# Performance work log

Measured on AMD Instinct MI355X. Metric: run time of the kernel, lower is better.

Reference implementation:

```python
import jax, jax.numpy as jnp
import numpy as np

# Dimensions
B, S, F, PATCH, D, H, NL, DFF, HOR = 512, 336, 12, 6, 512, 8, 6, 2048, 24
NP = S // PATCH        # 56 temporal patches
DH = D // H            # head dim = 64
EPS = 1e-5


def layer_norm(x, g, b):
    m = jnp.mean(x, axis=-1, keepdims=True)
    v = jnp.mean(jnp.square(x - m), axis=-1, keepdims=True)
    return (x - m) * jax.lax.rsqrt(v + EPS) * g + b


def alibi_bias(n_heads, n):
    # slopes = 2^(-8h/H), h = 1..H (standard ALiBi, H power of 2)
    slopes = 2.0 ** (-8.0 * jnp.arange(1, n_heads + 1, dtype=jnp.float32) / n_heads)
    pos = jnp.arange(n, dtype=jnp.float32)
    dist = jnp.abs(pos[:, None] - pos[None, :])         # [n, n]
    return -slopes[:, None, None] * dist                # [H, n, n]


def setup_inputs() -> dict:
    key = jax.random.key(0)
    ks = jax.random.split(key, 16)
    g = lambda k, shape: jax.random.normal(k, shape, dtype=jnp.float32) * 0.02
    return {
        "x": jax.random.normal(ks[0], (B, S, F), dtype=jnp.float32),
        "patch_W": g(ks[1], (PATCH * F, D)),
        "patch_b": jnp.zeros((D,), jnp.float32),
        "pos": g(ks[2], (NP, D)),
        "ln1_g": jnp.ones((NL, D), jnp.float32),
        "ln1_b": jnp.zeros((NL, D), jnp.float32),
        "Wq": g(ks[3], (NL, D, D)), "bq": jnp.zeros((NL, D), jnp.float32),
        "Wk": g(ks[4], (NL, D, D)), "bk": jnp.zeros((NL, D), jnp.float32),
        "Wv": g(ks[5], (NL, D, D)), "bv": jnp.zeros((NL, D), jnp.float32),
        "Wo": g(ks[6], (NL, D, D)), "bo": jnp.zeros((NL, D), jnp.float32),
        "ln2_g": jnp.ones((NL, D), jnp.float32),
        "ln2_b": jnp.zeros((NL, D), jnp.float32),
        "W1": g(ks[7], (NL, D, DFF)), "b1": jnp.zeros((NL, DFF), jnp.float32),
        "W2": g(ks[8], (NL, DFF, D)), "b2": jnp.zeros((NL, D), jnp.float32),
        "fn_g": jnp.ones((D,), jnp.float32),
        "fn_b": jnp.zeros((D,), jnp.float32),
        "head_W": g(ks[9], (D, HOR)),
        "head_b": jnp.zeros((HOR,), jnp.float32),
    }


def reference(x, patch_W, patch_b, pos, ln1_g, ln1_b, Wq, bq, Wk, bk, Wv, bv,
              Wo, bo, ln2_g, ln2_b, W1, b1, W2, b2, fn_g, fn_b, head_W, head_b):
    # Temporal patch embedding: (B,S,F) -> (B,NP,PATCH*F) -> Linear -> +pos
    h = x.reshape(B, NP, PATCH * F) @ patch_W + patch_b + pos  # [B, NP, D]
    bias = alibi_bias(H, NP)                                   # [H, NP, NP]
    scale = 1.0 / np.sqrt(DH).astype(np.float32)
    for l in range(NL):
        # Pre-LN multi-head attention with ALiBi temporal decay bias
        hn = layer_norm(h, ln1_g[l], ln1_b[l])
        q = (hn @ Wq[l] + bq[l]).reshape(B, NP, H, DH)
        k = (hn @ Wk[l] + bk[l]).reshape(B, NP, H, DH)
        v = (hn @ Wv[l] + bv[l]).reshape(B, NP, H, DH)
        sc = jnp.einsum('bqhd,bkhd->bhqk', q, k) * scale + bias[None]
        a = jax.nn.softmax(sc, axis=-1)
        o = jnp.einsum('bhqk,bkhd->bqhd', a, v).reshape(B, NP, D)
        h = h + (o @ Wo[l] + bo[l])
        # Pre-LN feedforward
        hn2 = layer_norm(h, ln2_g[l], ln2_b[l])
        h = h + (jax.nn.gelu(hn2 @ W1[l] + b1[l]) @ W2[l] + b2[l])
    pooled = jnp.mean(h, axis=1)                               # [B, D]
    out = layer_norm(pooled, fn_g, fn_b) @ head_W + head_b     # [B, HOR]
    return out
```

## Files before the change

### kernel.cpp

```cpp
#include <hip/hip_runtime.h>
#include <hip/hip_bf16.h>
#include <math.h>

#define D_      512
#define NPATCH  56
#define DFF_    2048
#define NLAYER  6
#define HEADS   8
#define DH_     64
#define HOR_    24
#define BATCH_  512
#define NTOK_   (BATCH_ * NPATCH)
#define KPAD    96

typedef __hip_bfloat16 bf16;
typedef __bf16 bf16x8 __attribute__((ext_vector_type(8)));
typedef float  f32x4  __attribute__((ext_vector_type(4)));

__device__ __forceinline__ void gload_lds16(const void* g, void* lds) {
    __builtin_amdgcn_global_load_lds(
        (const __attribute__((address_space(1))) unsigned int*)g,
        (__attribute__((address_space(3))) unsigned int*)lds, 16, 0, 0);
}

__device__ __forceinline__ float block_sum256(float v) {
    __shared__ float sm[4];
    const int lane = threadIdx.x & 63;
    const int w    = threadIdx.x >> 6;
    #pragma unroll
    for (int o = 32; o > 0; o >>= 1) v += __shfl_down(v, o);
    __syncthreads();
    if (lane == 0) sm[w] = v;
    __syncthreads();
    return sm[0] + sm[1] + sm[2] + sm[3];
}

__device__ __forceinline__ float gelu_fast(float xg) {
    const float e = __expf(1.5957691216057308f * (xg + 0.044715f * xg * xg * xg));
    return xg - xg * __builtin_amdgcn_rcpf(1.f + e);
}

__global__ __launch_bounds__(256) void transpose_bf16_k(
    const float* __restrict__ in, bf16* __restrict__ out, int R, int C,
    size_t in_ls, size_t out_ls)
{
    __shared__ float t[32][33];
    in  += (size_t)blockIdx.z * in_ls;
    out += (size_t)blockIdx.z * out_ls;
    const int c0 = blockIdx.x * 32, r0 = blockIdx.y * 32;
    const int x = threadIdx.x & 31, y = threadIdx.x >> 5;
    #pragma unroll
    for (int i = 0; i < 4; i++)
        t[y + i * 8][x] = in[(size_t)(r0 + y + i * 8) * C + c0 + x];
    __syncthreads();
    #pragma unroll
    for (int i = 0; i < 4; i++)
        out[(size_t)(c0 + y + i * 8) * R + r0 + x] = __float2bfloat16(t[x][y + i * 8]);
}

__global__ __launch_bounds__(256) void pwt_k(
    const float* __restrict__ W, bf16* __restrict__ out)
{
    const int idx = blockIdx.x * 256 + threadIdx.x;
    if (idx >= D_ * KPAD) return;
    const int n = idx / KPAD, kk = idx % KPAD;
    out[idx] = (kk < 72) ? __float2bfloat16(W[kk * D_ + n]) : __float2bfloat16(0.f);
}

__global__ __launch_bounds__(256) void xpad_k(
    const float* __restrict__ x, bf16* __restrict__ out)
{
    const size_t idx = (size_t)blockIdx.x * 256 + threadIdx.x;
    if (idx >= (size_t)NTOK_ * KPAD) return;
    const size_t row = idx / KPAD;
    const int kk = (int)(idx - row * KPAD);
    out[idx] = (kk < 72) ? __float2bfloat16(x[row * 72 + kk]) : __float2bfloat16(0.f);
}

__global__ __launch_bounds__(256) void bqkv_k(
    const float* __restrict__ bq, const float* __restrict__ bk,
    const float* __restrict__ bv, float* __restrict__ o)
{
    const int idx = blockIdx.x * 256 + threadIdx.x;
    if (idx >= NLAYER * 3 * D_) return;
    const int l = idx / (3 * D_), n = idx % (3 * D_);
    float v;
    if      (n < D_)     v = bq[l * D_ + n];
    else if (n < 2 * D_) v = bk[l * D_ + n - D_];
    else                 v = bv[l * D_ + n - 2 * D_];
    o[idx] = v;
}

__global__ __launch_bounds__(256) void layernorm_bf16_k(
    const bf16* __restrict__ x, const float* __restrict__ g,
    const float* __restrict__ b, bf16* __restrict__ y)
{
    const int w = threadIdx.x >> 6, lane = threadIdx.x & 63;
    const size_t row = (size_t)blockIdx.x * 4 + w;
    const bf16x8 a8 = *(const bf16x8*)((const __bf16*)x + row * D_ + lane * 8);
    float a[8];
    #pragma unroll
    for (int i = 0; i < 8; i++) a[i] = (float)a8[i];
    float s = 0.f;
    #pragma unroll
    for (int i = 0; i < 8; i++) s += a[i];
    #pragma unroll
    for (int o = 32; o > 0; o >>= 1) s += __shfl_xor(s, o);
    const float mean = s * (1.f / 512.f);
    float d[8];
    #pragma unroll
    for (int i = 0; i < 8; i++) d[i] = a[i] - mean;
    float v = 0.f;
    #pragma unroll
    for (int i = 0; i < 8; i++) v += d[i] * d[i];
    #pragma unroll
    for (int o = 32; o > 0; o >>= 1) v += __shfl_xor(v, o);
    const float rstd = rsqrtf(v * (1.f / 512.f) + 1e-5f);
    const float4 g0 = *(const float4*)(g + lane * 8);
    const float4 g1 = *(const float4*)(g + lane * 8 + 4);
    const float4 b0 = *(const float4*)(b + lane * 8);
    const float4 b1 = *(const float4*)(b + lane * 8 + 4);
    const float gg[8] = {g0.x, g0.y, g0.z, g0.w, g1.x, g1.y, g1.z, g1.w};
    const float bb[8] = {b0.x, b0.y, b0.z, b0.w, b1.x, b1.y, b1.z, b1.w};
    bf16x8 o8;
    #pragma unroll
    for (int i = 0; i < 8; i++) o8[i] = (__bf16)(d[i] * rstd * gg[i] + bb[i]);
    *(bf16x8*)((__bf16*)y + row * D_ + lane * 8) = o8;
}

template<bool GELU, bool RESID, bool POS, bool QKVSPLIT>
__global__ __launch_bounds__(256, 2) void gemm_bf16_k(
    const bf16* __restrict__ A, const bf16* __restrict__ Bt,
    const float* __restrict__ bias, const bf16* __restrict__ resid,
    const float* __restrict__ pos, bf16* __restrict__ Cp,
    bf16* __restrict__ vt, int M, int N, int K, int nx)
{
    __shared__ __align__(16) bf16 As[3][128 * 32];
    __shared__ __align__(16) bf16 Bs[3][256 * 32];
    const int tid  = threadIdx.x;
    const int wid  = tid >> 6;
    const int lane = tid & 63;

    const int nwg = gridDim.x;
    const int q8 = nwg >> 3, r8 = nwg & 7;
    const int xcd = blockIdx.x & 7, idx8 = blockIdx.x >> 3;
    const int swz = (xcd < r8 ? xcd * (q8 + 1) : r8 * (q8 + 1) + (xcd - r8) * q8) + idx8;
    const int n0 = (swz % nx) * 256;
    const int m0 = (swz / nx) * 128;
    const int wr = wid >> 1, wc = wid & 1;

    f32x4 acc[4][8];
    #pragma unroll
    for (int m = 0; m < 4; m++)
        #pragma unroll
        for (int n = 0; n < 8; n++) acc[m][n] = f32x4{0.f, 0.f, 0.f, 0.f};

    const int srow = lane >> 2;
    const int schunk = ((lane & 3) ^ ((lane >> 3) & 3)) * 8;
    const bf16* gA = A  + (size_t)(m0 + wid * 32 + srow) * K + schunk;
    const bf16* gB = Bt + (size_t)(n0 + wid * 64 + srow) * K + schunk;
    const size_t k16 = (size_t)16 * K;
    const int sa0 = (wid * 2) * 512;
    const int sb0 = (wid * 4) * 512;

    const int fr = lane & 15;
    const int qg = lane >> 4;
    const int roff = fr * 32 + ((qg ^ ((fr >> 1) & 3)) * 8);

    const int nt = K >> 5;
    #define STAGE(buf, kt)  do { const bf16* _a = gA + ((kt) << 5);              \
        const bf16* _b = gB + ((kt) << 5);                                       \
        gload_lds16(_a,            &As[buf][sa0]);                               \
        gload_lds16(_a + k16,      &As[buf][sa0 + 512]);                         \
        gload_lds16(_b,            &Bs[buf][sb0]);                               \
        gload_lds16(_b + k16,      &Bs[buf][sb0 + 512]);                         \
        gload_lds16(_b + 2 * k16,  &Bs[buf][sb0 + 1024]);                        \
        gload_lds16(_b + 3 * k16,  &Bs[buf][sb0 + 1536]); } while (0)

    STAGE(0, 0);
    STAGE(1, 1);

    int cur = 0, nxt = 2;
    for (int t = 0; t < nt; t++) {
        if (t < nt - 1) asm volatile("s_waitcnt vmcnt(6)" ::: "memory");
        else            asm volatile("s_waitcnt vmcnt(0)" ::: "memory");
        __builtin_amdgcn_s_barrier();
        __builtin_amdgcn_sched_barrier(0);
        bf16x8 af[4], bg[8];
        #pragma unroll
        for (int m = 0; m < 4; m++) af[m] = *(const bf16x8*)&As[cur][(wr * 4 + m) * 512 + roff];
        #pragma unroll
        for (int n = 0; n < 8; n++) bg[n] = *(const bf16x8*)&Bs[cur][(wc * 8 + n) * 512 + roff];
        if (t + 2 < nt) STAGE(nxt, t + 2);
        #pragma unroll
        for (int m = 0; m < 4; m++)
            #pragma unroll
            for (int n = 0; n < 8; n++)
                acc[m][n] = __builtin_amdgcn_mfma_f32_16x16x32_bf16(af[m], bg[n], acc[m][n], 0, 0, 0);
        cur = (cur == 2) ? 0 : cur + 1;
        nxt = (nxt == 2) ? 0 : nxt + 1;
    }
    #undef STAGE

    const int rq = qg * 4;
    #pragma unroll
    for (int m = 0; m < 4; m++) {
        #pragma unroll
        for (int n = 0; n < 8; n++) {
            const int col = n0 + wc * 128 + n * 16 + fr;
            const float bcol = bias[col];
            #pragma unroll
            for (int j = 0; j < 4; j++) {
                const int row = m0 + wr * 64 + m * 16 + rq + j;
                float c = acc[m][n][j] + bcol;
                if (GELU)  c = gelu_fast(c);
                if (RESID) c += __bfloat162float(resid[(size_t)row * N + col]);
                if (POS)   c += pos[(size_t)(row % NPATCH) * D_ + col];
                if (QKVSPLIT) {
                    if (col < 1024) {
                        Cp[(size_t)row * 1024 + col] = __float2bfloat16(c);
                    } else {
                        const int c2 = col - 1024, hh = c2 >> 6, dd = c2 & 63;
                        const int bb = row / NPATCH, pp = row - bb * NPATCH;
                        vt[(((size_t)bb * 8 + hh) * 64 + dd) * 64 + pp] = __float2bfloat16(c);
                    }
                } else {
                    Cp[(size_t)row * N + col] = __float2bfloat16(c);
                }
            }
        }
    }
}

__global__ __launch_bounds__(256) void attn_mfma_k(
    const bf16* __restrict__ qk, const bf16* __restrict__ vt,
    bf16* __restrict__ ao)
{
    __shared__ __align__(16) bf16 St[4][64 * 72];
    const int tid  = threadIdx.x;
    const int w    = tid >> 6, lane = tid & 63;
    const int bh   = blockIdx.x * 4 + w;
    const int b    = bh >> 3, hh = bh & 7;
    const int fr   = lane & 15;
    const int qg   = lane >> 4;
    const int kc   = qg * 8;

    const bf16* Qb = qk + (size_t)b * NPATCH * 1024 + hh * 64;
    const bf16* Kb = Qb + 512;
    const bf16* Vb = vt + (size_t)bh * 4096;

    bf16x8 qf[4][2], kf[4][2];
    #pragma unroll
    for (int m = 0; m < 4; m++)
        #pragma unroll
        for (int ks = 0; ks < 2; ks++) {
            qf[m][ks] = *(const bf16x8*)&Qb[(size_t)(m * 16 + fr) * 1024 + ks * 32 + kc];
            kf[m][ks] = *(const bf16x8*)&Kb[(size_t)(m * 16 + fr) * 1024 + ks * 32 + kc];
        }

    f32x4 acc[4][4];
    #pragma unroll
    for (int m = 0; m < 4; m++)
        #pragma unroll
        for (int n = 0; n < 4; n++) acc[m][n] = f32x4{0.f, 0.f, 0.f, 0.f};
    #pragma unroll
    for (int ks = 0; ks < 2; ks++)
        #pragma unroll
        for (int m = 0; m < 4; m++)
            #pragma unroll
            for (int n = 0; n < 4; n++)
                acc[m][n] = __builtin_amdgcn_mfma_f32_16x16x32_bf16(qf[m][ks], kf[n][ks], acc[m][n], 0, 0, 0);

    bf16x8 vf[4][2];
    #pragma unroll
    for (int n = 0; n < 4; n++)
        #pragma unroll
        for (int ks = 0; ks < 2; ks++)
            vf[n][ks] = *(const bf16x8*)&Vb[(size_t)(n * 16 + fr) * 64 + ks * 32 + kc];

    const float slope = exp2f(-(float)(hh + 1));
    bf16* Sw = St[w];
    #pragma unroll
    for (int m = 0; m < 4; m++) {
        #pragma unroll
        for (int j = 0; j < 4; j++) {
            const int r = m * 16 + qg * 4 + j;
            float s[4];
            #pragma unroll
            for (int n = 0; n < 4; n++) {
                const int col = n * 16 + fr;
                float sv = acc[m][n][j] * 0.125f - slope * fabsf((float)(r - col));
                s[n] = (col >= NPATCH) ? -1e30f : sv;
            }
            float mx = fmaxf(fmaxf(s[0], s[1]), fmaxf(s[2], s[3]));
            mx = fmaxf(mx, __shfl_xor(mx, 1));
            mx = fmaxf(mx, __shfl_xor(mx, 2));
            mx = fmaxf(mx, __shfl_xor(mx, 4));
            mx = fmaxf(mx, __shfl_xor(mx, 8));
            float p[4], sum = 0.f;
            #pragma unroll
            for (int n = 0; n < 4; n++) { p[n] = __expf(s[n] - mx); sum += p[n]; }
            sum += __shfl_xor(sum, 1);
            sum += __shfl_xor(sum, 2);
            sum += __shfl_xor(sum, 4);
            sum += __shfl_xor(sum, 8);
            const float inv = 1.f / sum;
            #pragma unroll
            for (int n = 0; n < 4; n++)
                Sw[r * 72 + n * 16 + fr] = __float2bfloat16(p[n] * inv);
        }
    }

    #pragma unroll
    for (int m = 0; m < 4; m++)
        #pragma unroll
        for (int n = 0; n < 4; n++) acc[m][n] = f32x4{0.f, 0.f, 0.f, 0.f};
    #pragma unroll
    for (int m = 0; m < 4; m++)
        #pragma unroll
        for (int ks = 0; ks < 2; ks++) {
            const bf16x8 pf = *(const bf16x8*)&Sw[(m * 16 + fr) * 72 + ks * 32 + kc];
            #pragma unroll
            for (int n = 0; n < 4; n++)
                acc[m][n] = __builtin_amdgcn_mfma_f32_16x16x32_bf16(pf, vf[n][ks], acc[m][n], 0, 0, 0);
        }

    bf16* Ob = ao + (size_t)b * NPATCH * 512 + hh * 64;
    #pragma unroll
    for (int m = 0; m < 4; m++)
        #pragma unroll
        for (int j = 0; j < 4; j++) {
            const int r = m * 16 + qg * 4 + j;
            if (r < NPATCH)
                #pragma unroll
                for (int n = 0; n < 4; n++)
                    Ob[(size_t)r * 512 + n * 16 + fr] = __float2bfloat16(acc[m][n][j]);
        }
}

__global__ __launch_bounds__(256) void head_k(
    const bf16* __restrict__ h, const float* __restrict__ g,
    const float* __restrict__ bb, const float* __restrict__ hW,
    const float* __restrict__ hb, float* __restrict__ out)
{
    const int b = blockIdx.x;
    __shared__ float row[D_];
    const int tid = threadIdx.x;
    float v0 = 0.f, v1 = 0.f;
    #pragma unroll
    for (int p = 0; p < NPATCH; p++) {
        const bf16* hr = h + (size_t)b * NPATCH * D_ + (size_t)p * D_;
        v0 += __bfloat162float(hr[tid]);
        v1 += __bfloat162float(hr[tid + 256]);
    }
    v0 *= (1.f / (float)NPATCH);
    v1 *= (1.f / (float)NPATCH);
    const float mean = block_sum256(v0 + v1) * (1.f / 512.f);
    const float d0 = v0 - mean, d1 = v1 - mean;
    const float var = block_sum256(d0 * d0 + d1 * d1) * (1.f / 512.f);
    const float rstd = rsqrtf(var + 1e-5f);
    row[tid]       = d0 * rstd * g[tid]       + bb[tid];
    row[tid + 256] = d1 * rstd * g[tid + 256] + bb[tid + 256];
    __syncthreads();
    if (tid < HOR_) {
        float acc = hb[tid];
        for (int kk = 0; kk < D_; kk++) acc = fmaf(row[kk], hW[kk * HOR_ + tid], acc);
        out[(size_t)b * HOR_ + tid] = acc;
    }
}

extern "C" void kernel_launch(void* const* d_in, const int* in_sizes, int n_in,
                              void* d_out, int out_size, void* d_ws, size_t ws_size,
                              hipStream_t stream)
{
    const float* x       = (const float*)d_in[0];
    const float* patch_W = (const float*)d_in[1];
    const float* patch_b = (const float*)d_in[2];
    const float* pos     = (const float*)d_in[3];
    const float* ln1_g   = (const float*)d_in[4];
    const float* ln1_b   = (const float*)d_in[5];
    const float* Wq      = (const float*)d_in[6];
    const float* bq      = (const float*)d_in[7];
    const float* Wk      = (const float*)d_in[8];
    const float* bk      = (const float*)d_in[9];
    const float* Wv      = (const float*)d_in[10];
    const float* bv      = (const float*)d_in[11];
    const float* Wo      = (const float*)d_in[12];
    const float* bo      = (const float*)d_in[13];
    const float* ln2_g   = (const float*)d_in[14];
    const float* ln2_b   = (const float*)d_in[15];
    const float* W1      = (const float*)d_in[16];
    const float* b1      = (const float*)d_in[17];
    const float* W2      = (const float*)d_in[18];
    const float* b2      = (const float*)d_in[19];
    const float* fn_g    = (const float*)d_in[20];
    const float* fn_b    = (const float*)d_in[21];
    const float* head_W  = (const float*)d_in[22];
    const float* head_b  = (const float*)d_in[23];
    float* out = (float*)d_out;

    const size_t WELEM  = (size_t)D_ * D_;
    const size_t WFELEM = (size_t)D_ * DFF_;
    bf16* wqkvt = (bf16*)d_ws;
    bf16* wot   = wqkvt + (size_t)NLAYER * 3 * WELEM;
    bf16* w1t   = wot   + (size_t)NLAYER * WELEM;
    bf16* w2t   = w1t   + (size_t)NLAYER * WFELEM;
    bf16* pwt   = w2t   + (size_t)NLAYER * WFELEM;
    float* bqkv = (float*)(pwt + (size_t)D_ * KPAD);
    bf16* xpad  = (bf16*)(bqkv + NLAYER * 3 * D_);
    char* wend  = (char*)(xpad + (size_t)NTOK_ * KPAD);
    const size_t FIXED = (size_t)(wend - (char*)d_ws);

    int BC = 16;
    for (int cand = BATCH_; cand >= 16; cand >>= 1) {
        const size_t need = FIXED + (size_t)cand * (56 * 5120 + 65536);
        if (need <= ws_size) { BC = cand; break; }
    }
    const int nChunks = BATCH_ / BC;
    const int CT = BC * NPATCH;
    const size_t TD = (size_t)CT * D_;

    bf16* h    = (bf16*)wend;
    bf16* hn   = h + TD;
    bf16* qk   = hn + TD;
    bf16* ao   = qk + (size_t)CT * 1024;
    bf16* vt   = ao + TD;
    bf16* mid  = qk;

    transpose_bf16_k<<<dim3(16, 16, NLAYER), 256, 0, stream>>>(
        Wq, wqkvt,                 D_, D_, WELEM, 3 * WELEM);
    transpose_bf16_k<<<dim3(16, 16, NLAYER), 256, 0, stream>>>(
        Wk, wqkvt + WELEM,         D_, D_, WELEM, 3 * WELEM);
    transpose_bf16_k<<<dim3(16, 16, NLAYER), 256, 0, stream>>>(
        Wv, wqkvt + 2 * WELEM,     D_, D_, WELEM, 3 * WELEM);
    transpose_bf16_k<<<dim3(16, 16, NLAYER), 256, 0, stream>>>(
        Wo, wot,                   D_, D_, WELEM, WELEM);
    transpose_bf16_k<<<dim3(64, 16, NLAYER), 256, 0, stream>>>(
        W1, w1t,                   D_, DFF_, WFELEM, WFELEM);
    transpose_bf16_k<<<dim3(16, 64, NLAYER), 256, 0, stream>>>(
        W2, w2t,                   DFF_, D_, WFELEM, WFELEM);
    pwt_k<<<(D_ * KPAD + 255) / 256, 256, 0, stream>>>(patch_W, pwt);
    bqkv_k<<<(NLAYER * 3 * D_ + 255) / 256, 256, 0, stream>>>(bq, bk, bv, bqkv);
    xpad_k<<<((size_t)NTOK_ * KPAD + 255) / 256, 256, 0, stream>>>(x, xpad);

    const int mt  = CT / 128;
    const int g1n = (D_ / 256) * mt;
    const int gqn = (3 * D_ / 256) * mt;
    const int g2n = (DFF_ / 256) * mt;

    for (int c = 0; c < nChunks; c++) {
        const size_t tok0 = (size_t)c * CT;

        gemm_bf16_k<false, false, true, false><<<g1n, 256, 0, stream>>>(
            xpad + tok0 * KPAD, pwt, patch_b, nullptr, pos, h, nullptr,
            CT, D_, KPAD, D_ / 256);

        for (int l = 0; l < NLAYER; l++) {
            layernorm_bf16_k<<<CT / 4, 256, 0, stream>>>(h, ln1_g + l * D_, ln1_b + l * D_, hn);
            gemm_bf16_k<false, false, false, true><<<gqn, 256, 0, stream>>>(
                hn, wqkvt + (size_t)l * 3 * WELEM, bqkv + l * 3 * D_, nullptr, nullptr,
                qk, vt, CT, 3 * D_, D_, 3 * D_ / 256);
            attn_mfma_k<<<BC * 2, 256, 0, stream>>>(qk, vt, ao);
            gemm_bf16_k<false, true, false, false><<<g1n, 256, 0, stream>>>(
                ao, wot + (size_t)l * WELEM, bo + l * D_, h, nullptr, h, nullptr,
                CT, D_, D_, D_ / 256);
            layernorm_bf16_k<<<CT / 4, 256, 0, stream>>>(h, ln2_g + l * D_, ln2_b + l * D_, hn);
            gemm_bf16_k<true, false, false, false><<<g2n, 256, 0, stream>>>(
                hn, w1t + (size_t)l * WFELEM, b1 + l * DFF_, nullptr, nullptr,
                mid, nullptr, CT, DFF_, D_, DFF_ / 256);
            gemm_bf16_k<false, true, false, false><<<g1n, 256, 0, stream>>>(
                mid, w2t + (size_t)l * WFELEM, b2 + l * D_, h, nullptr, h, nullptr,
                CT, D_, DFF_, D_ / 256);
        }

        head_k<<<BC, 256, 0, stream>>>(h, fn_g, fn_b, head_W, head_b,
                                       out + (size_t)c * BC * HOR_);
    }
}
```

Measured before the change: 2.004 ms.

## Use 8-wave GEMM workgroups with 64x64 warp tiles and unified LDS staging

The GEMM goes from 4 waves to 8 waves per 128x256 block. Each wave now computes a 64x64 sub-tile instead of 64x128, which halves the accumulator registers per wave. The A and B tiles are merged into one LDS buffer, and each wave issues 3 async global-to-LDS loads per stage instead of 6. The goal is more resident waves for latency hiding; the cost is lower per-wave operand reuse from LDS and more LDS read traffic relative to MFMA work.

```diff
diff --git a/kernel.cpp b/kernel.cpp
--- a/kernel.cpp
+++ b/kernel.cpp
@@ -129,14 +129,13 @@
 }
 
 template<bool GELU, bool RESID, bool POS, bool QKVSPLIT>
-__global__ __launch_bounds__(256, 2) void gemm_bf16_k(
+__global__ __launch_bounds__(512, 4) void gemm_bf16_k(
     const bf16* __restrict__ A, const bf16* __restrict__ Bt,
     const float* __restrict__ bias, const bf16* __restrict__ resid,
     const float* __restrict__ pos, bf16* __restrict__ Cp,
     bf16* __restrict__ vt, int M, int N, int K, int nx)
 {
-    __shared__ __align__(16) bf16 As[3][128 * 32];
-    __shared__ __align__(16) bf16 Bs[3][256 * 32];
+    __shared__ __align__(16) bf16 ABs[3][384 * 32];
     const int tid  = threadIdx.x;
     const int wid  = tid >> 6;
     const int lane = tid & 63;
@@ -147,55 +146,58 @@
     const int swz = (xcd < r8 ? xcd * (q8 + 1) : r8 * (q8 + 1) + (xcd - r8) * q8) + idx8;
     const int n0 = (swz % nx) * 256;
     const int m0 = (swz / nx) * 128;
-    const int wr = wid >> 1, wc = wid & 1;
-
-    f32x4 acc[4][8];
-    #pragma unroll
-    for (int m = 0; m < 4; m++)
-        #pragma unroll
-        for (int n = 0; n < 8; n++) acc[m][n] = f32x4{0.f, 0.f, 0.f, 0.f};
+    const int wr = wid >> 2, wc = wid & 3;
+
+    f32x4 acc[4][4];
+    #pragma unroll
+    for (int m = 0; m < 4; m++)
+        #pragma unroll
+        for (int n = 0; n < 4; n++) acc[m][n] = f32x4{0.f, 0.f, 0.f, 0.f};
 
     const int srow = lane >> 2;
     const int schunk = ((lane & 3) ^ ((lane >> 3) & 3)) * 8;
-    const bf16* gA = A  + (size_t)(m0 + wid * 32 + srow) * K + schunk;
-    const bf16* gB = Bt + (size_t)(n0 + wid * 64 + srow) * K + schunk;
-    const size_t k16 = (size_t)16 * K;
-    const int sa0 = (wid * 2) * 512;
-    const int sb0 = (wid * 4) * 512;
+    const bf16* sp[3];
+    int soff[3];
+    #pragma unroll
+    for (int i = 0; i < 3; i++) {
+        const int s = wid * 3 + i;
+        soff[i] = s * 512;
+        sp[i] = (s < 8)
+            ? A  + (size_t)(m0 + s * 16 + srow) * K + schunk
+            : Bt + (size_t)(n0 + (s - 8) * 16 + srow) * K + schunk;
+    }
 
     const int fr = lane & 15;
     const int qg = lane >> 4;
     const int roff = fr * 32 + ((qg ^ ((fr >> 1) & 3)) * 8);
 
     const int nt = K >> 5;
-    #define STAGE(buf, kt)  do { const bf16* _a = gA + ((kt) << 5);              \
-        const bf16* _b = gB + ((kt) << 5);                                       \
-        gload_lds16(_a,            &As[buf][sa0]);                               \
-        gload_lds16(_a + k16,      &As[buf][sa0 + 512]);                         \
-        gload_lds16(_b,            &Bs[buf][sb0]);                               \
-        gload_lds16(_b + k16,      &Bs[buf][sb0 + 512]);                         \
-        gload_lds16(_b + 2 * k16,  &Bs[buf][sb0 + 1024]);                        \
-        gload_lds16(_b + 3 * k16,  &Bs[buf][sb0 + 1536]); } while (0)
+    #define STAGE(buf, kt)  do {                                   \
+        gload_lds16(sp[0] + ((kt) << 5), &ABs[buf][soff[0]]);      \
+        gload_lds16(sp[1] + ((kt) << 5), &ABs[buf][soff[1]]);      \
+        gload_lds16(sp[2] + ((kt) << 5), &ABs[buf][soff[2]]); } while (0)
 
     STAGE(0, 0);
     STAGE(1, 1);
 
     int cur = 0, nxt = 2;
     for (int t = 0; t < nt; t++) {
-        if (t < nt - 1) asm volatile("s_waitcnt vmcnt(6)" ::: "memory");
+        if (t < nt - 1) asm volatile("s_waitcnt vmcnt(3)" ::: "memory");
         else            asm volatile("s_waitcnt vmcnt(0)" ::: "memory");
         __builtin_amdgcn_s_barrier();
         __builtin_amdgcn_sched_barrier(0);
-        bf16x8 af[4], bg[8];
-        #pragma unroll
-        for (int m = 0; m < 4; m++) af[m] = *(const bf16x8*)&As[cur][(wr * 4 + m) * 512 + roff];
-        #pragma unroll
-        for (int n = 0; n < 8; n++) bg[n] = *(const bf16x8*)&Bs[cur][(wc * 8 + n) * 512 + roff];
+        bf16x8 af[4], bg[4];
+        #pragma unroll
+        for (int m = 0; m < 4; m++)
+            af[m] = *(const bf16x8*)&ABs[cur][(wr * 4 + m) * 512 + roff];
+        #pragma unroll
+        for (int n = 0; n < 4; n++)
+            bg[n] = *(const bf16x8*)&ABs[cur][(8 + wc * 4 + n) * 512 + roff];
         if (t + 2 < nt) STAGE(nxt, t + 2);
         #pragma unroll
         for (int m = 0; m < 4; m++)
             #pragma unroll
-            for (int n = 0; n < 8; n++)
+            for (int n = 0; n < 4; n++)
                 acc[m][n] = __builtin_amdgcn_mfma_f32_16x16x32_bf16(af[m], bg[n], acc[m][n], 0, 0, 0);
         cur = (cur == 2) ? 0 : cur + 1;
         nxt = (nxt == 2) ? 0 : nxt + 1;
@@ -206,8 +208,8 @@
     #pragma unroll
     for (int m = 0; m < 4; m++) {
         #pragma unroll
-        for (int n = 0; n < 8; n++) {
-            const int col = n0 + wc * 128 + n * 16 + fr;
+        for (int n = 0; n < 4; n++) {
+            const int col = n0 + wc * 64 + n * 16 + fr;
             const float bcol = bias[col];
             #pragma unroll
             for (int j = 0; j < 4; j++) {
@@ -451,24 +453,24 @@
     for (int c = 0; c < nChunks; c++) {
         const size_t tok0 = (size_t)c * CT;
 
-        gemm_bf16_k<false, false, true, false><<<g1n, 256, 0, stream>>>(
+        gemm_bf16_k<false, false, true, false><<<g1n, 512, 0, stream>>>(
             xpad + tok0 * KPAD, pwt, patch_b, nullptr, pos, h, nullptr,
             CT, D_, KPAD, D_ / 256);
 
         for (int l = 0; l < NLAYER; l++) {
             layernorm_bf16_k<<<CT / 4, 256, 0, stream>>>(h, ln1_g + l * D_, ln1_b + l * D_, hn);
-            gemm_bf16_k<false, false, false, true><<<gqn, 256, 0, stream>>>(
+            gemm_bf16_k<false, false, false, true><<<gqn, 512, 0, stream>>>(
                 hn, wqkvt + (size_t)l * 3 * WELEM, bqkv + l * 3 * D_, nullptr, nullptr,
                 qk, vt, CT, 3 * D_, D_, 3 * D_ / 256);
             attn_mfma_k<<<BC * 2, 256, 0, stream>>>(qk, vt, ao);
-            gemm_bf16_k<false, true, false, false><<<g1n, 256, 0, stream>>>(
+            gemm_bf16_k<false, true, false, false><<<g1n, 512, 0, stream>>>(
                 ao, wot + (size_t)l * WELEM, bo + l * D_, h, nullptr, h, nullptr,
                 CT, D_, D_, D_ / 256);
             layernorm_bf16_k<<<CT / 4, 256, 0, stream>>>(h, ln2_g + l * D_, ln2_b + l * D_, hn);
-            gemm_bf16_k<true, false, false, false><<<g2n, 256, 0, stream>>>(
+            gemm_bf16_k<true, false, false, false><<<g2n, 512, 0, stream>>>(
                 hn, w1t + (size_t)l * WFELEM, b1 + l * DFF_, nullptr, nullptr,
                 mid, nullptr, CT, DFF_, D_, DFF_ / 256);
-            gemm_bf16_k<false, true, false, false><<<g1n, 256, 0, stream>>>(
+            gemm_bf16_k<false, true, false, false><<<g1n, 512, 0, stream>>>(
                 mid, w2t + (size_t)l * WFELEM, b2 + l * D_, h, nullptr, h, nullptr,
                 CT, D_, DFF_, D_ / 256);
         }
```

Result: no change. 1.977 ms (-1.3%).
